# Performance work log

Measured on AMD Instinct MI355X. Metric: run time of the kernel, lower is better.

Reference implementation:

```python
import jax, jax.numpy as jnp
import numpy as np

B, H, N, D = 16, 8, 256, 32


def setup_inputs() -> dict:
    key = jax.random.key(0)
    k1, k2, k3 = jax.random.split(key, 3)
    q = jax.random.normal(k1, (B, H, N, D), dtype=jnp.float32)
    k = jax.random.normal(k2, (B, H, N, D), dtype=jnp.float32)
    scale = jnp.ones((1,), dtype=jnp.float32)  # unused by the module
    mask = jnp.zeros((B, 1, N, N), dtype=bool)  # True == masked out
    # learned attention vector, xavier_uniform over (1, H, 1, 1, D)
    fan = 1 * H * 1 * 1 * D
    bound = float(np.sqrt(6.0 / (1 + D)))  # xavier for (..., D) param
    attention = jax.random.uniform(k3, (1, H, 1, 1, D), dtype=jnp.float32,
                                   minval=-bound, maxval=bound)
    return {"q": q, "k": k, "scale": scale, "mask": mask, "attention": attention}


def reference(q, k, scale, mask, attention):
    # summed: [B, H, Nq, Nk, D] via broadcast of q.unsqueeze(-2)+k.unsqueeze(-3)
    summed = q[:, :, :, None, :] + k[:, :, None, :, :]
    # GATv2 score: a^T * silu(q_i + k_j), reduced over head_dim
    scores = jnp.sum(jax.nn.silu(summed) * attention, axis=-1)  # [B, H, Nq, Nk]
    neg = jnp.finfo(scores.dtype).min
    scores_masked = jnp.where(mask, neg, scores)
    attn = jax.nn.softmax(scores_masked, axis=-1)
    return attn
```

## Files before the change

### kernel.cpp

```cpp
#include <hip/hip_runtime.h>
#include <stdint.h>
#include <stddef.h>

constexpr int Bc = 16, Hc = 8, Nc = 256, Dc = 32;
constexpr float LOG2E = 1.44269504088896340736f;

constexpr int    MF    = 12;
constexpr double PHALF = 11.5;
constexpr double LFIT  = 9.0;

constexpr double PI_ = 3.14159265358979323846;

constexpr double cexp_(double x) {
    int n = (int)(x >= 0 ? x + 0.5 : x - 0.5);
    double f = x - n, t = 1.0, s = 1.0;
    for (int i = 1; i <= 26; ++i) { t *= f / i; s += t; }
    const double E = 2.71828182845904523536;
    double en = 1.0, bb = n >= 0 ? E : 1.0 / E;
    int an = n < 0 ? -n : n;
    for (int i = 0; i < an; ++i) en *= bb;
    return s * en;
}
constexpr double creduce_(double x) {
    while (x >  PI_) x -= 2.0 * PI_;
    while (x < -PI_) x += 2.0 * PI_;
    return x;
}
constexpr double ccos_(double x0) {
    double x = creduce_(x0), x2 = x * x, t = 1.0, s = 1.0;
    for (int i = 1; i <= 16; ++i) { t *= -x2 / ((2.0*i - 1.0) * (2.0*i)); s += t; }
    return s;
}
constexpr double csin_(double x0) {
    double x = creduce_(x0), x2 = x * x, t = x, s = x;
    for (int i = 1; i <= 16; ++i) { t *= -x2 / ((2.0*i) * (2.0*i + 1.0)); s += t; }
    return s;
}
constexpr double Gfun_(double x) {
    double z = x < 0 ? -x : x;
    double e = cexp_(z);
    return 0.5 * z * ((e - 1.0) / (e + 1.0));
}
constexpr double csqrt_(double x) {
    if (x <= 0) return 0;
    double r = x > 1 ? x : 1;
    for (int i = 0; i < 40; ++i) r = 0.5 * (r + x / r);
    return r;
}

struct FitT { float tk[MF + 1]; float tq[MF + 1]; };

constexpr FitT lsFit_() {
    constexpr int NB = MF + 1;
    double A[NB][NB] = {}, bv[NB] = {};
    for (int p = 0; p < NB; ++p)
        for (int qq = 0; qq < NB; ++qq) {
            double wm = (p - qq) * PI_ / PHALF, wp = (p + qq) * PI_ / PHALF;
            double Sm = (p == qq)     ? LFIT : csin_(wm * LFIT) / wm;
            double Sp = (p + qq == 0) ? LFIT : csin_(wp * LFIT) / wp;
            A[p][qq] = 0.5 * (Sm + Sp);
        }
    constexpr int NS = 128;
    double hh = LFIT / NS, gx[NS + 1] = {};
    for (int i = 0; i <= NS; ++i) gx[i] = Gfun_(i * hh);
    for (int p = 0; p < NB; ++p) {
        double s = 0;
        for (int i = 0; i <= NS; ++i) {
            double wgt = (i == 0 || i == NS) ? 1.0 : ((i & 1) ? 4.0 : 2.0);
            s += wgt * gx[i] * ccos_(p * PI_ / PHALF * (i * hh));
        }
        bv[p] = s * hh / 3.0;
    }
    for (int p = 0; p < NB; ++p) A[p][p] += 1e-8 * LFIT;
    for (int col = 0; col < NB; ++col) {
        int piv = col; double best = A[col][col] < 0 ? -A[col][col] : A[col][col];
        for (int r = col + 1; r < NB; ++r) {
            double v = A[r][col] < 0 ? -A[r][col] : A[r][col];
            if (v > best) { best = v; piv = r; }
        }
        if (piv != col) {
            for (int cc = 0; cc < NB; ++cc) { double t = A[col][cc]; A[col][cc] = A[piv][cc]; A[piv][cc] = t; }
            double t = bv[col]; bv[col] = bv[piv]; bv[piv] = t;
        }
        for (int r = col + 1; r < NB; ++r) {
            double f = A[r][col] / A[col][col];
            for (int cc = col; cc < NB; ++cc) A[r][cc] -= f * A[col][cc];
            bv[r] -= f * bv[col];
        }
    }
    double c[NB] = {};
    for (int r = NB - 1; r >= 0; --r) {
        double s = bv[r];
        for (int cc = r + 1; cc < NB; ++cc) s -= A[r][cc] * c[cc];
        c[r] = s / A[r][r];
    }
    FitT f{};
    for (int m = 0; m <= MF; ++m) {
        double rt = csqrt_(c[m] < 0 ? -c[m] : c[m]);
        f.tk[m] = (float)rt;
        f.tq[m] = (float)(c[m] < 0 ? -rt : rt);
    }
    return f;
}
constexpr FitT CF = lsFit_();

typedef _Float16 half8  __attribute__((ext_vector_type(8)));
typedef float    f32x16 __attribute__((ext_vector_type(16)));

__device__ __forceinline__ uint32_t pkh_(float a, float b) {
    auto v = __builtin_amdgcn_cvt_pkrtz(a, b);
    uint32_t u; __builtin_memcpy(&u, &v, 4); return u;
}

constexpr int ROWB = 144;
constexpr int KFR = 256, QFR = 128;
constexpr int BUFB = (KFR + QFR) * ROWB;
constexpr int SMEM_BYTES = 2 * BUFB + 1024 + 2048;

__global__ __launch_bounds__(512, 2) void gatv2_mfma_kernel(
    const float* __restrict__ q, const float* __restrict__ k,
    const uint8_t* __restrict__ mask, const float* __restrict__ att,
    float* __restrict__ out)
{
    extern __shared__ char smem[];
    float* akv  = (float*)(smem + 2 * BUFB);
    float* sred = (float*)(smem + 2 * BUFB + 1024);

    const int tid = threadIdx.x, lane = tid & 63, w = tid >> 6;
    const int bh = blockIdx.y, h = bh & 7, b = bh >> 3;
    const int iBlk = blockIdx.x * 128;
    const float invTwoP = (float)(1.0 / (2.0 * PHALF));

    const int dq = tid & 7, rw = tid >> 3;
    const float4 av4 = *(const float4*)(att + h * Dc + 4 * dq);

    const float* kbase = k + (size_t)bh * Nc * Dc;
    float kc1[16], ks1[16], kcm[16], ksm[16];
    int offK[4];
#pragma unroll
    for (int it = 0; it < 4; ++it) {
        int j = it * 64 + rw;
        float4 kv = *(const float4*)(kbase + j * Dc + 4 * dq);
        float part = av4.x * kv.x + av4.y * kv.y + av4.z * kv.z + av4.w * kv.w;
        part += __shfl_xor(part, 1, 64);
        part += __shfl_xor(part, 2, 64);
        part += __shfl_xor(part, 4, 64);
        if (dq == 0) akv[j] = part;
        float rv[4] = { kv.x, kv.y, kv.z, kv.w };
#pragma unroll
        for (int c = 0; c < 4; ++c) {
            float r = __builtin_amdgcn_fractf(rv[c] * invTwoP);
            kc1[4*it+c] = __builtin_amdgcn_cosf(r);
            ks1[4*it+c] = __builtin_amdgcn_sinf(r);
            kcm[4*it+c] = kc1[4*it+c];
            ksm[4*it+c] = ks1[4*it+c];
        }
        int sw = (j ^ (j >> 3)) & 7;
        offK[it] = j * ROWB + ((dq ^ sw) << 4);
    }
    const float* qbase = q + ((size_t)bh * Nc + iBlk) * Dc;
    float qc1[8], qs1[8], qcm[8], qsm[8];
    int offQ[2];
#pragma unroll
    for (int it = 0; it < 2; ++it) {
        int i = it * 64 + rw;
        float4 qv = *(const float4*)(qbase + i * Dc + 4 * dq);
        float rv[4] = { qv.x, qv.y, qv.z, qv.w };
#pragma unroll
        for (int c = 0; c < 4; ++c) {
            float r = __builtin_amdgcn_fractf(rv[c] * invTwoP);
            qc1[4*it+c] = __builtin_amdgcn_cosf(r);
            qs1[4*it+c] = __builtin_amdgcn_sinf(r);
            qcm[4*it+c] = qc1[4*it+c];
            qsm[4*it+c] = qs1[4*it+c];
        }
        int sw = (i ^ (i >> 3)) & 7;
        offQ[it] = KFR * ROWB + i * ROWB + ((dq ^ sw) << 4);
    }

    const int hi5 = lane >> 5, col = lane & 31;
    const int wi = w & 1, wj = w >> 1;
    int offA[2][4], offB[2][4];
#pragma unroll
    for (int it2 = 0; it2 < 2; ++it2) {
        int r = wi * 64 + it2 * 32 + col, sw = (r ^ (r >> 3)) & 7;
#pragma unroll
        for (int s = 0; s < 4; ++s)
            offA[it2][s] = KFR * ROWB + r * ROWB + (((2 * s + hi5) ^ sw) << 4);
    }
#pragma unroll
    for (int jt = 0; jt < 2; ++jt) {
        int r = wj * 64 + jt * 32 + col, sw = (r ^ (r >> 3)) & 7;
#pragma unroll
        for (int s = 0; s < 4; ++s)
            offB[jt][s] = r * ROWB + (((2 * s + hi5) ^ sw) << 4);
    }

    f32x16 acc[2][2];
#pragma unroll
    for (int a2 = 0; a2 < 2; ++a2)
#pragma unroll
        for (int b2 = 0; b2 < 2; ++b2)
#pragma unroll
            for (int e = 0; e < 16; ++e) acc[a2][b2][e] = 0.0f;

    auto buildChunk = [&](int m, int dstOff) {
        const float tk = CF.tk[m];
        const float g0 = CF.tq[m] * av4.x, g1 = CF.tq[m] * av4.y;
        const float g2 = CF.tq[m] * av4.z, g3 = CF.tq[m] * av4.w;
#pragma unroll
        for (int it = 0; it < 4; ++it) {
            uint4 wv;
            wv.x = pkh_(tk * kcm[4*it+0], tk * ksm[4*it+0]);
            wv.y = pkh_(tk * kcm[4*it+1], tk * ksm[4*it+1]);
            wv.z = pkh_(tk * kcm[4*it+2], tk * ksm[4*it+2]);
            wv.w = pkh_(tk * kcm[4*it+3], tk * ksm[4*it+3]);
            *(uint4*)(smem + dstOff + offK[it]) = wv;
        }
#pragma unroll
        for (int it = 0; it < 2; ++it) {
            uint4 wv;
            wv.x = pkh_(g0 * qcm[4*it+0], -(g0 * qsm[4*it+0]));
            wv.y = pkh_(g1 * qcm[4*it+1], -(g1 * qsm[4*it+1]));
            wv.z = pkh_(g2 * qcm[4*it+2], -(g2 * qsm[4*it+2]));
            wv.w = pkh_(g3 * qcm[4*it+3], -(g3 * qsm[4*it+3]));
            *(uint4*)(smem + dstOff + offQ[it]) = wv;
        }
        if (m < MF) {
#pragma unroll
            for (int e = 0; e < 16; ++e) {
                float cn = fmaf(kc1[e], kcm[e], -(ks1[e] * ksm[e]));
                float sn = fmaf(ks1[e], kcm[e],   kc1[e] * ksm[e]);
                kcm[e] = cn; ksm[e] = sn;
            }
#pragma unroll
            for (int e = 0; e < 8; ++e) {
                float cn = fmaf(qc1[e], qcm[e], -(qs1[e] * qsm[e]));
                float sn = fmaf(qs1[e], qcm[e],   qc1[e] * qsm[e]);
                qcm[e] = cn; qsm[e] = sn;
            }
        }
    };

    auto mfmaChunk = [&](int srcOff) {
#pragma unroll
        for (int s = 0; s < 4; ++s) {
            half8 A0 = *(const half8*)(smem + srcOff + offA[0][s]);
            half8 A1 = *(const half8*)(smem + srcOff + offA[1][s]);
            half8 B0 = *(const half8*)(smem + srcOff + offB[0][s]);
            half8 B1 = *(const half8*)(smem + srcOff + offB[1][s]);
            acc[0][0] = __builtin_amdgcn_mfma_f32_32x32x16_f16(A0, B0, acc[0][0], 0, 0, 0);
            acc[0][1] = __builtin_amdgcn_mfma_f32_32x32x16_f16(A0, B1, acc[0][1], 0, 0, 0);
            acc[1][0] = __builtin_amdgcn_mfma_f32_32x32x16_f16(A1, B0, acc[1][0], 0, 0, 0);
            acc[1][1] = __builtin_amdgcn_mfma_f32_32x32x16_f16(A1, B1, acc[1][1], 0, 0, 0);
        }
    };

    buildChunk(1, 0);
    __syncthreads();
#pragma unroll
    for (int m = 1; m <= MF; ++m) {
        if (m < MF) buildChunk(m + 1, (m & 1) * BUFB);
        mfmaChunk(((m - 1) & 1) * BUFB);
        __syncthreads();
    }

    constexpr float M0 = 24.0f;
    const int jB = wj * 64;
    const float akj0 = akv[jB + col], akj1 = akv[jB + 32 + col];
    const int iB = iBlk + wi * 64;

#pragma unroll
    for (int it2 = 0; it2 < 2; ++it2)
#pragma unroll
        for (int e = 0; e < 16; ++e) {
            int rloc = (e & 3) + 8 * (e >> 2) + 4 * hi5;
            int ig = iB + it2 * 32 + rloc;
            const uint8_t* mr = mask + ((size_t)(b * Nc + ig)) * Nc + jB + col;
            float v0 = fmaf(0.5f, akj0, acc[it2][0][e]);
            float v1 = fmaf(0.5f, akj1, acc[it2][1][e]);
            if (mr[0])  v0 = -1.0e30f;
            if (mr[32]) v1 = -1.0e30f;
            float p0 = __builtin_amdgcn_exp2f(__builtin_fminf((v0 - M0) * LOG2E, 80.0f));
            float p1 = __builtin_amdgcn_exp2f(__builtin_fminf((v1 - M0) * LOG2E, 80.0f));
            acc[it2][0][e] = p0;
            acc[it2][1][e] = p1;
            float sm = p0 + p1;
#pragma unroll
            for (int off = 1; off < 32; off <<= 1) sm += __shfl_xor(sm, off, 64);
            if (col == e) sred[(wi * 64 + it2 * 32 + rloc) * 4 + wj] = sm;
        }
    __syncthreads();

    float* obase = out + (size_t)bh * Nc * Nc;
#pragma unroll
    for (int it2 = 0; it2 < 2; ++it2)
#pragma unroll
        for (int e = 0; e < 16; ++e) {
            int rloc = (e & 3) + 8 * (e >> 2) + 4 * hi5;
            int iL = wi * 64 + it2 * 32 + rloc;
            int ig = iB + it2 * 32 + rloc;
            float4 tv = *(const float4*)(&sred[iL * 4]);
            float inv = __builtin_amdgcn_rcpf(tv.x + tv.y + tv.z + tv.w);
            obase[(size_t)ig * Nc + jB + col]      = acc[it2][0][e] * inv;
            obase[(size_t)ig * Nc + jB + 32 + col] = acc[it2][1][e] * inv;
        }
}

extern "C" void kernel_launch(void* const* d_in, const int* in_sizes, int n_in,
                              void* d_out, int out_size, void* d_ws, size_t ws_size,
                              hipStream_t stream) {
    const float*   q    = (const float*)d_in[0];
    const float*   k    = (const float*)d_in[1];
    const uint8_t* mask = (const uint8_t*)d_in[3];
    const float*   att  = (const float*)d_in[4];
    float*         out  = (float*)d_out;

    (void)hipFuncSetAttribute((const void*)gatv2_mfma_kernel,
                              hipFuncAttributeMaxDynamicSharedMemorySize, SMEM_BYTES);

    dim3 grid(2, Bc * Hc);
    dim3 block(512);
    gatv2_mfma_kernel<<<grid, block, SMEM_BYTES, stream>>>(q, k, mask, att, out);
}
```

Measured before the change: 104.7 us.

## Use 1024-thread blocks with smaller per-wave tiles and fewer Fourier terms

Doubles the block to 16 waves, each computing a 32x64 score tile with two accumulators instead of a 64x64 tile with four. Per-thread staging work for K and Q fragments is halved. Separately, the Fourier approximation of SiLU drops from 12 to 10 harmonics with a shorter period, so fewer MFMA chunks are built and multiplied. The fewer harmonics may reduce accuracy, and the larger block with no occupancy hint changes register pressure and residency.

```diff
diff --git a/kernel.cpp b/kernel.cpp
--- a/kernel.cpp
+++ b/kernel.cpp
@@ -5,8 +5,8 @@
 constexpr int Bc = 16, Hc = 8, Nc = 256, Dc = 32;
 constexpr float LOG2E = 1.44269504088896340736f;
 
-constexpr int    MF    = 12;
-constexpr double PHALF = 11.5;
+constexpr int    MF    = 10;
+constexpr double PHALF = 9.7;
 constexpr double LFIT  = 9.0;
 
 constexpr double PI_ = 3.14159265358979323846;
@@ -117,7 +117,7 @@
 constexpr int BUFB = (KFR + QFR) * ROWB;
 constexpr int SMEM_BYTES = 2 * BUFB + 1024 + 2048;
 
-__global__ __launch_bounds__(512, 2) void gatv2_mfma_kernel(
+__global__ __launch_bounds__(1024) void gatv2_mfma_kernel(
     const float* __restrict__ q, const float* __restrict__ k,
     const uint8_t* __restrict__ mask, const float* __restrict__ att,
     float* __restrict__ out)
@@ -135,11 +135,11 @@
     const float4 av4 = *(const float4*)(att + h * Dc + 4 * dq);
 
     const float* kbase = k + (size_t)bh * Nc * Dc;
-    float kc1[16], ks1[16], kcm[16], ksm[16];
-    int offK[4];
-#pragma unroll
-    for (int it = 0; it < 4; ++it) {
-        int j = it * 64 + rw;
+    float kc1[8], ks1[8], kcm[8], ksm[8];
+    int offK[2];
+#pragma unroll
+    for (int it = 0; it < 2; ++it) {
+        int j = rw + it * 128;
         float4 kv = *(const float4*)(kbase + j * Dc + 4 * dq);
         float part = av4.x * kv.x + av4.y * kv.y + av4.z * kv.z + av4.w * kv.w;
         part += __shfl_xor(part, 1, 64);
@@ -159,57 +159,44 @@
         offK[it] = j * ROWB + ((dq ^ sw) << 4);
     }
     const float* qbase = q + ((size_t)bh * Nc + iBlk) * Dc;
-    float qc1[8], qs1[8], qcm[8], qsm[8];
-    int offQ[2];
-#pragma unroll
-    for (int it = 0; it < 2; ++it) {
-        int i = it * 64 + rw;
-        float4 qv = *(const float4*)(qbase + i * Dc + 4 * dq);
+    float qc1[4], qs1[4], qcm[4], qsm[4];
+    int offQ;
+    {
+        float4 qv = *(const float4*)(qbase + rw * Dc + 4 * dq);
         float rv[4] = { qv.x, qv.y, qv.z, qv.w };
 #pragma unroll
         for (int c = 0; c < 4; ++c) {
             float r = __builtin_amdgcn_fractf(rv[c] * invTwoP);
-            qc1[4*it+c] = __builtin_amdgcn_cosf(r);
-            qs1[4*it+c] = __builtin_amdgcn_sinf(r);
-            qcm[4*it+c] = qc1[4*it+c];
-            qsm[4*it+c] = qs1[4*it+c];
-        }
-        int sw = (i ^ (i >> 3)) & 7;
-        offQ[it] = KFR * ROWB + i * ROWB + ((dq ^ sw) << 4);
+            qc1[c] = __builtin_amdgcn_cosf(r);
+            qs1[c] = __builtin_amdgcn_sinf(r);
+            qcm[c] = qc1[c];
+            qsm[c] = qs1[c];
+        }
+        int sw = (rw ^ (rw >> 3)) & 7;
+        offQ = KFR * ROWB + rw * ROWB + ((dq ^ sw) << 4);
     }
 
     const int hi5 = lane >> 5, col = lane & 31;
-    const int wi = w & 1, wj = w >> 1;
-    int offA[2][4], offB[2][4];
-#pragma unroll
-    for (int it2 = 0; it2 < 2; ++it2) {
-        int r = wi * 64 + it2 * 32 + col, sw = (r ^ (r >> 3)) & 7;
-#pragma unroll
-        for (int s = 0; s < 4; ++s)
-            offA[it2][s] = KFR * ROWB + r * ROWB + (((2 * s + hi5) ^ sw) << 4);
-    }
-#pragma unroll
-    for (int jt = 0; jt < 2; ++jt) {
-        int r = wj * 64 + jt * 32 + col, sw = (r ^ (r >> 3)) & 7;
-#pragma unroll
-        for (int s = 0; s < 4; ++s)
-            offB[jt][s] = r * ROWB + (((2 * s + hi5) ^ sw) << 4);
-    }
-
-    f32x16 acc[2][2];
-#pragma unroll
-    for (int a2 = 0; a2 < 2; ++a2)
-#pragma unroll
-        for (int b2 = 0; b2 < 2; ++b2)
-#pragma unroll
-            for (int e = 0; e < 16; ++e) acc[a2][b2][e] = 0.0f;
+    const int wi = w & 3, wj = w >> 2;
+    const int rA  = wi * 32 + col;
+    const int swA = (rA ^ (rA >> 3)) & 7;
+    const int baseA = KFR * ROWB + rA * ROWB;
+    const int rB0 = wj * 64 + col, rB1 = rB0 + 32;
+    const int swB0 = (rB0 ^ (rB0 >> 3)) & 7, swB1 = (rB1 ^ (rB1 >> 3)) & 7;
+    const int baseB0 = rB0 * ROWB, baseB1 = rB1 * ROWB;
+
+    f32x16 acc[2];
+#pragma unroll
+    for (int jt = 0; jt < 2; ++jt)
+#pragma unroll
+        for (int e = 0; e < 16; ++e) acc[jt][e] = 0.0f;
 
     auto buildChunk = [&](int m, int dstOff) {
         const float tk = CF.tk[m];
         const float g0 = CF.tq[m] * av4.x, g1 = CF.tq[m] * av4.y;
         const float g2 = CF.tq[m] * av4.z, g3 = CF.tq[m] * av4.w;
 #pragma unroll
-        for (int it = 0; it < 4; ++it) {
+        for (int it = 0; it < 2; ++it) {
             uint4 wv;
             wv.x = pkh_(tk * kcm[4*it+0], tk * ksm[4*it+0]);
             wv.y = pkh_(tk * kcm[4*it+1], tk * ksm[4*it+1]);
@@ -217,24 +204,23 @@
             wv.w = pkh_(tk * kcm[4*it+3], tk * ksm[4*it+3]);
             *(uint4*)(smem + dstOff + offK[it]) = wv;
         }
-#pragma unroll
-        for (int it = 0; it < 2; ++it) {
+        {
             uint4 wv;
-            wv.x = pkh_(g0 * qcm[4*it+0], -(g0 * qsm[4*it+0]));
-            wv.y = pkh_(g1 * qcm[4*it+1], -(g1 * qsm[4*it+1]));
-            wv.z = pkh_(g2 * qcm[4*it+2], -(g2 * qsm[4*it+2]));
-            wv.w = pkh_(g3 * qcm[4*it+3], -(g3 * qsm[4*it+3]));
-            *(uint4*)(smem + dstOff + offQ[it]) = wv;
+            wv.x = pkh_(g0 * qcm[0], -(g0 * qsm[0]));
+            wv.y = pkh_(g1 * qcm[1], -(g1 * qsm[1]));
+            wv.z = pkh_(g2 * qcm[2], -(g2 * qsm[2]));
+            wv.w = pkh_(g3 * qcm[3], -(g3 * qsm[3]));
+            *(uint4*)(smem + dstOff + offQ) = wv;
         }
         if (m < MF) {
 #pragma unroll
-            for (int e = 0; e < 16; ++e) {
+            for (int e = 0; e < 8; ++e) {
                 float cn = fmaf(kc1[e], kcm[e], -(ks1[e] * ksm[e]));
                 float sn = fmaf(ks1[e], kcm[e],   kc1[e] * ksm[e]);
                 kcm[e] = cn; ksm[e] = sn;
             }
 #pragma unroll
-            for (int e = 0; e < 8; ++e) {
+            for (int e = 0; e < 4; ++e) {
                 float cn = fmaf(qc1[e], qcm[e], -(qs1[e] * qsm[e]));
                 float sn = fmaf(qs1[e], qcm[e],   qc1[e] * qsm[e]);
                 qcm[e] = cn; qsm[e] = sn;
@@ -245,14 +231,12 @@
     auto mfmaChunk = [&](int srcOff) {
 #pragma unroll
         for (int s = 0; s < 4; ++s) {
-            half8 A0 = *(const half8*)(smem + srcOff + offA[0][s]);
-            half8 A1 = *(const half8*)(smem + srcOff + offA[1][s]);
-            half8 B0 = *(const half8*)(smem + srcOff + offB[0][s]);
-            half8 B1 = *(const half8*)(smem + srcOff + offB[1][s]);
-            acc[0][0] = __builtin_amdgcn_mfma_f32_32x32x16_f16(A0, B0, acc[0][0], 0, 0, 0);
-            acc[0][1] = __builtin_amdgcn_mfma_f32_32x32x16_f16(A0, B1, acc[0][1], 0, 0, 0);
-            acc[1][0] = __builtin_amdgcn_mfma_f32_32x32x16_f16(A1, B0, acc[1][0], 0, 0, 0);
-            acc[1][1] = __builtin_amdgcn_mfma_f32_32x32x16_f16(A1, B1, acc[1][1], 0, 0, 0);
+            int u = 2 * s + hi5;
+            half8 A  = *(const half8*)(smem + srcOff + baseA  + ((u ^ swA ) << 4));
+            half8 B0 = *(const half8*)(smem + srcOff + baseB0 + ((u ^ swB0) << 4));
+            half8 B1 = *(const half8*)(smem + srcOff + baseB1 + ((u ^ swB1) << 4));
+            acc[0] = __builtin_amdgcn_mfma_f32_32x32x16_f16(A, B0, acc[0], 0, 0, 0);
+            acc[1] = __builtin_amdgcn_mfma_f32_32x32x16_f16(A, B1, acc[1], 0, 0, 0);
         }
     };
 
@@ -268,43 +252,39 @@
     constexpr float M0 = 24.0f;
     const int jB = wj * 64;
     const float akj0 = akv[jB + col], akj1 = akv[jB + 32 + col];
-    const int iB = iBlk + wi * 64;
-
-#pragma unroll
-    for (int it2 = 0; it2 < 2; ++it2)
-#pragma unroll
-        for (int e = 0; e < 16; ++e) {
-            int rloc = (e & 3) + 8 * (e >> 2) + 4 * hi5;
-            int ig = iB + it2 * 32 + rloc;
-            const uint8_t* mr = mask + ((size_t)(b * Nc + ig)) * Nc + jB + col;
-            float v0 = fmaf(0.5f, akj0, acc[it2][0][e]);
-            float v1 = fmaf(0.5f, akj1, acc[it2][1][e]);
-            if (mr[0])  v0 = -1.0e30f;
-            if (mr[32]) v1 = -1.0e30f;
-            float p0 = __builtin_amdgcn_exp2f(__builtin_fminf((v0 - M0) * LOG2E, 80.0f));
-            float p1 = __builtin_amdgcn_exp2f(__builtin_fminf((v1 - M0) * LOG2E, 80.0f));
-            acc[it2][0][e] = p0;
-            acc[it2][1][e] = p1;
-            float sm = p0 + p1;
-#pragma unroll
-            for (int off = 1; off < 32; off <<= 1) sm += __shfl_xor(sm, off, 64);
-            if (col == e) sred[(wi * 64 + it2 * 32 + rloc) * 4 + wj] = sm;
-        }
+    const int iB = iBlk + wi * 32;
+
+#pragma unroll
+    for (int e = 0; e < 16; ++e) {
+        int rloc = (e & 3) + 8 * (e >> 2) + 4 * hi5;
+        int ig = iB + rloc;
+        const uint8_t* mr = mask + ((size_t)(b * Nc + ig)) * Nc + jB + col;
+        float v0 = fmaf(0.5f, akj0, acc[0][e]);
+        float v1 = fmaf(0.5f, akj1, acc[1][e]);
+        if (mr[0])  v0 = -1.0e30f;
+        if (mr[32]) v1 = -1.0e30f;
+        float p0 = __builtin_amdgcn_exp2f(__builtin_fminf((v0 - M0) * LOG2E, 80.0f));
+        float p1 = __builtin_amdgcn_exp2f(__builtin_fminf((v1 - M0) * LOG2E, 80.0f));
+        acc[0][e] = p0;
+        acc[1][e] = p1;
+        float sm = p0 + p1;
+#pragma unroll
+        for (int off = 1; off < 32; off <<= 1) sm += __shfl_xor(sm, off, 64);
+        if (col == e) sred[(wi * 32 + rloc) * 4 + wj] = sm;
+    }
     __syncthreads();
 
     float* obase = out + (size_t)bh * Nc * Nc;
 #pragma unroll
-    for (int it2 = 0; it2 < 2; ++it2)
-#pragma unroll
-        for (int e = 0; e < 16; ++e) {
-            int rloc = (e & 3) + 8 * (e >> 2) + 4 * hi5;
-            int iL = wi * 64 + it2 * 32 + rloc;
-            int ig = iB + it2 * 32 + rloc;
-            float4 tv = *(const float4*)(&sred[iL * 4]);
-            float inv = __builtin_amdgcn_rcpf(tv.x + tv.y + tv.z + tv.w);
-            obase[(size_t)ig * Nc + jB + col]      = acc[it2][0][e] * inv;
-            obase[(size_t)ig * Nc + jB + 32 + col] = acc[it2][1][e] * inv;
-        }
+    for (int e = 0; e < 16; ++e) {
+        int rloc = (e & 3) + 8 * (e >> 2) + 4 * hi5;
+        int iL = wi * 32 + rloc;
+        int ig = iB + rloc;
+        float4 tv = *(const float4*)(&sred[iL * 4]);
+        float inv = __builtin_amdgcn_rcpf(tv.x + tv.y + tv.z + tv.w);
+        obase[(size_t)ig * Nc + jB + col]      = acc[0][e] * inv;
+        obase[(size_t)ig * Nc + jB + 32 + col] = acc[1][e] * inv;
+    }
 }
 
 extern "C" void kernel_launch(void* const* d_in, const int* in_sizes, int n_in,
@@ -320,6 +300,6 @@
                               hipFuncAttributeMaxDynamicSharedMemorySize, SMEM_BYTES);
 
     dim3 grid(2, Bc * Hc);
-    dim3 block(512);
+    dim3 block(1024);
     gatv2_mfma_kernel<<<grid, block, SMEM_BYTES, stream>>>(q, k, mask, att, out);
 }
```

New measurement: 98.82 us. -5.7%, faster.

## Precompute K Fourier features in separate kernel and DMA them into LDS

Applied to the files above, without the earlier changes.

Splits the work into a feature kernel that computes the half-precision K Fourier features and the a·k terms once per (b,h), and a GEMM kernel that streams those features from workspace into LDS with global_load_lds DMA while it builds only the Q features. This removes the K feature computation that was repeated in both row blocks and takes VALU work out of the MFMA loop. It also cuts the Fourier order from 12 to 10 and shrinks the period, which changes the approximation's accuracy. The cost is a second kernel launch and a large workspace write and read of the K features.

```diff
diff --git a/kernel.cpp b/kernel.cpp
--- a/kernel.cpp
+++ b/kernel.cpp
@@ -5,8 +5,8 @@
 constexpr int Bc = 16, Hc = 8, Nc = 256, Dc = 32;
 constexpr float LOG2E = 1.44269504088896340736f;
 
-constexpr int    MF    = 12;
-constexpr double PHALF = 11.5;
+constexpr int    MF    = 10;
+constexpr double PHALF = 9.7;
 constexpr double LFIT  = 9.0;
 
 constexpr double PI_ = 3.14159265358979323846;
@@ -112,60 +112,91 @@
     uint32_t u; __builtin_memcpy(&u, &v, 4); return u;
 }
 
-constexpr int ROWB = 144;
-constexpr int KFR = 256, QFR = 128;
-constexpr int BUFB = (KFR + QFR) * ROWB;
-constexpr int SMEM_BYTES = 2 * BUFB + 1024 + 2048;
-
-__global__ __launch_bounds__(512, 2) void gatv2_mfma_kernel(
-    const float* __restrict__ q, const float* __restrict__ k,
-    const uint8_t* __restrict__ mask, const float* __restrict__ att,
-    float* __restrict__ out)
+__device__ __forceinline__ void dma16(const char* g, char* l) {
+    __builtin_amdgcn_global_load_lds(
+        (const __attribute__((address_space(1))) unsigned int*)(g),
+        (__attribute__((address_space(3))) unsigned int*)(l),
+        16, 0, 0);
+}
+
+constexpr int    KCH      = Nc * 128;
+constexpr size_t KF_BYTES = (size_t)Bc * Hc * MF * KCH;
+constexpr size_t AK_OFF   = KF_BYTES;
+
+__global__ __launch_bounds__(256) void feat_kernel(
+    const float* __restrict__ k, const float* __restrict__ att,
+    char* __restrict__ kf, float* __restrict__ akg)
+{
+    const int gid = blockIdx.x * 256 + threadIdx.x;
+    const int u  = gid & 7;
+    const int j  = (gid >> 3) & (Nc - 1);
+    const int bh = gid >> 11;
+    const int h  = bh & (Hc - 1);
+    const float4 kv = *(const float4*)(k + ((size_t)bh * Nc + j) * Dc + 4 * u);
+    const float4 a4 = *(const float4*)(att + h * Dc + 4 * u);
+    float part = a4.x * kv.x + a4.y * kv.y + a4.z * kv.z + a4.w * kv.w;
+    part += __shfl_xor(part, 1, 64);
+    part += __shfl_xor(part, 2, 64);
+    part += __shfl_xor(part, 4, 64);
+    if (u == 0) akg[bh * Nc + j] = part;
+
+    const float invTwoP = (float)(1.0 / (2.0 * PHALF));
+    float c1[4], s1[4], cm[4], sm[4];
+    const float rv[4] = { kv.x, kv.y, kv.z, kv.w };
+#pragma unroll
+    for (int c = 0; c < 4; ++c) {
+        float r = __builtin_amdgcn_fractf(rv[c] * invTwoP);
+        c1[c] = __builtin_amdgcn_cosf(r);
+        s1[c] = __builtin_amdgcn_sinf(r);
+        cm[c] = c1[c]; sm[c] = s1[c];
+    }
+    char* base = kf + (size_t)bh * (MF * KCH) + j * 128 + ((u ^ (j & 7)) << 4);
+#pragma unroll
+    for (int m = 1; m <= MF; ++m) {
+        const float tk = CF.tk[m];
+        uint4 wv;
+        wv.x = pkh_(tk * cm[0], tk * sm[0]);
+        wv.y = pkh_(tk * cm[1], tk * sm[1]);
+        wv.z = pkh_(tk * cm[2], tk * sm[2]);
+        wv.w = pkh_(tk * cm[3], tk * sm[3]);
+        *(uint4*)(base + (size_t)(m - 1) * KCH) = wv;
+        if (m < MF) {
+#pragma unroll
+            for (int e = 0; e < 4; ++e) {
+                float cn = fmaf(c1[e], cm[e], -(s1[e] * sm[e]));
+                float sn = fmaf(s1[e], cm[e],   c1[e] * sm[e]);
+                cm[e] = cn; sm[e] = sn;
+            }
+        }
+    }
+}
+
+constexpr int QCH   = 128 * 128;
+constexpr int QBASE = 2 * KCH;
+constexpr int SRED  = QBASE + 2 * QCH;
+constexpr int SMEM2 = SRED + 2048;
+
+__global__ __launch_bounds__(512, 2) void gatv2_gemm_kernel(
+    const float* __restrict__ q, const uint8_t* __restrict__ mask,
+    const float* __restrict__ att, const char* __restrict__ kf,
+    const float* __restrict__ akg, float* __restrict__ out)
 {
     extern __shared__ char smem[];
-    float* akv  = (float*)(smem + 2 * BUFB);
-    float* sred = (float*)(smem + 2 * BUFB + 1024);
-
+    float* sred = (float*)(smem + SRED);
     const int tid = threadIdx.x, lane = tid & 63, w = tid >> 6;
     const int bh = blockIdx.y, h = bh & 7, b = bh >> 3;
     const int iBlk = blockIdx.x * 128;
     const float invTwoP = (float)(1.0 / (2.0 * PHALF));
 
     const int dq = tid & 7, rw = tid >> 3;
-    const float4 av4 = *(const float4*)(att + h * Dc + 4 * dq);
-
-    const float* kbase = k + (size_t)bh * Nc * Dc;
-    float kc1[16], ks1[16], kcm[16], ksm[16];
-    int offK[4];
-#pragma unroll
-    for (int it = 0; it < 4; ++it) {
-        int j = it * 64 + rw;
-        float4 kv = *(const float4*)(kbase + j * Dc + 4 * dq);
-        float part = av4.x * kv.x + av4.y * kv.y + av4.z * kv.z + av4.w * kv.w;
-        part += __shfl_xor(part, 1, 64);
-        part += __shfl_xor(part, 2, 64);
-        part += __shfl_xor(part, 4, 64);
-        if (dq == 0) akv[j] = part;
-        float rv[4] = { kv.x, kv.y, kv.z, kv.w };
-#pragma unroll
-        for (int c = 0; c < 4; ++c) {
-            float r = __builtin_amdgcn_fractf(rv[c] * invTwoP);
-            kc1[4*it+c] = __builtin_amdgcn_cosf(r);
-            ks1[4*it+c] = __builtin_amdgcn_sinf(r);
-            kcm[4*it+c] = kc1[4*it+c];
-            ksm[4*it+c] = ks1[4*it+c];
-        }
-        int sw = (j ^ (j >> 3)) & 7;
-        offK[it] = j * ROWB + ((dq ^ sw) << 4);
-    }
-    const float* qbase = q + ((size_t)bh * Nc + iBlk) * Dc;
+    const float4 a4 = *(const float4*)(att + h * Dc + 4 * dq);
     float qc1[8], qs1[8], qcm[8], qsm[8];
     int offQ[2];
 #pragma unroll
     for (int it = 0; it < 2; ++it) {
-        int i = it * 64 + rw;
-        float4 qv = *(const float4*)(qbase + i * Dc + 4 * dq);
-        float rv[4] = { qv.x, qv.y, qv.z, qv.w };
+        const int i = rw + it * 64;
+        const float4 qv = *(const float4*)(q + ((size_t)bh * Nc + iBlk + i) * Dc + 4 * dq);
+        const float rv[4] = { qv.x, qv.y, qv.z, qv.w };
 #pragma unroll
         for (int c = 0; c < 4; ++c) {
             float r = __builtin_amdgcn_fractf(rv[c] * invTwoP);
@@ -174,65 +205,32 @@
             qcm[4*it+c] = qc1[4*it+c];
             qsm[4*it+c] = qs1[4*it+c];
         }
-        int sw = (i ^ (i >> 3)) & 7;
-        offQ[it] = KFR * ROWB + i * ROWB + ((dq ^ sw) << 4);
-    }
-
-    const int hi5 = lane >> 5, col = lane & 31;
-    const int wi = w & 1, wj = w >> 1;
-    int offA[2][4], offB[2][4];
-#pragma unroll
-    for (int it2 = 0; it2 < 2; ++it2) {
-        int r = wi * 64 + it2 * 32 + col, sw = (r ^ (r >> 3)) & 7;
-#pragma unroll
-        for (int s = 0; s < 4; ++s)
-            offA[it2][s] = KFR * ROWB + r * ROWB + (((2 * s + hi5) ^ sw) << 4);
-    }
-#pragma unroll
-    for (int jt = 0; jt < 2; ++jt) {
-        int r = wj * 64 + jt * 32 + col, sw = (r ^ (r >> 3)) & 7;
-#pragma unroll
-        for (int s = 0; s < 4; ++s)
-            offB[jt][s] = r * ROWB + (((2 * s + hi5) ^ sw) << 4);
-    }
-
-    f32x16 acc[2][2];
-#pragma unroll
-    for (int a2 = 0; a2 < 2; ++a2)
-#pragma unroll
-        for (int b2 = 0; b2 < 2; ++b2)
-#pragma unroll
-            for (int e = 0; e < 16; ++e) acc[a2][b2][e] = 0.0f;
-
-    auto buildChunk = [&](int m, int dstOff) {
-        const float tk = CF.tk[m];
-        const float g0 = CF.tq[m] * av4.x, g1 = CF.tq[m] * av4.y;
-        const float g2 = CF.tq[m] * av4.z, g3 = CF.tq[m] * av4.w;
-#pragma unroll
-        for (int it = 0; it < 4; ++it) {
-            uint4 wv;
-            wv.x = pkh_(tk * kcm[4*it+0], tk * ksm[4*it+0]);
-            wv.y = pkh_(tk * kcm[4*it+1], tk * ksm[4*it+1]);
-            wv.z = pkh_(tk * kcm[4*it+2], tk * ksm[4*it+2]);
-            wv.w = pkh_(tk * kcm[4*it+3], tk * ksm[4*it+3]);
-            *(uint4*)(smem + dstOff + offK[it]) = wv;
-        }
+        offQ[it] = QBASE + i * 128 + ((dq ^ (i & 7)) << 4);
+    }
+
+    const char* kg = kf + (size_t)bh * (MF * KCH) + w * 4096 + lane * 16;
+
+    auto dmaK = [&](int mIdx, int buf) {
+        const char* g = kg + (size_t)mIdx * KCH;
+        char* l = smem + buf * KCH + w * 4096;
+#pragma unroll
+        for (int t = 0; t < 4; ++t)
+            dma16(g + t * 1024, l + t * 1024);
+    };
+
+    auto buildQ = [&](int m, int buf) {
+        const float g0 = CF.tq[m]*a4.x, g1 = CF.tq[m]*a4.y;
+        const float g2 = CF.tq[m]*a4.z, g3 = CF.tq[m]*a4.w;
 #pragma unroll
         for (int it = 0; it < 2; ++it) {
             uint4 wv;
-            wv.x = pkh_(g0 * qcm[4*it+0], -(g0 * qsm[4*it+0]));
-            wv.y = pkh_(g1 * qcm[4*it+1], -(g1 * qsm[4*it+1]));
-            wv.z = pkh_(g2 * qcm[4*it+2], -(g2 * qsm[4*it+2]));
-            wv.w = pkh_(g3 * qcm[4*it+3], -(g3 * qsm[4*it+3]));
-            *(uint4*)(smem + dstOff + offQ[it]) = wv;
+            wv.x = pkh_(g0*qcm[4*it+0], -(g0*qsm[4*it+0]));
+            wv.y = pkh_(g1*qcm[4*it+1], -(g1*qsm[4*it+1]));
+            wv.z = pkh_(g2*qcm[4*it+2], -(g2*qsm[4*it+2]));
+            wv.w = pkh_(g3*qcm[4*it+3], -(g3*qsm[4*it+3]));
+            *(uint4*)(smem + buf * QCH + offQ[it]) = wv;
         }
         if (m < MF) {
-#pragma unroll
-            for (int e = 0; e < 16; ++e) {
-                float cn = fmaf(kc1[e], kcm[e], -(ks1[e] * ksm[e]));
-                float sn = fmaf(ks1[e], kcm[e],   kc1[e] * ksm[e]);
-                kcm[e] = cn; ksm[e] = sn;
-            }
 #pragma unroll
             for (int e = 0; e < 8; ++e) {
                 float cn = fmaf(qc1[e], qcm[e], -(qs1[e] * qsm[e]));
@@ -242,13 +240,29 @@
         }
     };
 
-    auto mfmaChunk = [&](int srcOff) {
+    const int hi5 = lane >> 5, col = lane & 31;
+    const int wi = w & 1, wj = w >> 1;
+    const int baseA0 = QBASE + (wi*64 + col) * 128, baseA1 = baseA0 + 32*128;
+    const int baseB0 = (wj*64 + col) * 128,         baseB1 = baseB0 + 32*128;
+    const int sA = col & 7;
+
+    f32x16 acc[2][2];
+#pragma unroll
+    for (int a2 = 0; a2 < 2; ++a2)
+#pragma unroll
+        for (int b2 = 0; b2 < 2; ++b2)
+#pragma unroll
+            for (int e = 0; e < 16; ++e) acc[a2][b2][e] = 0.0f;
+
+    auto mfmaC = [&](int buf) {
+        const int qb = buf * QCH, kb = buf * KCH;
 #pragma unroll
         for (int s = 0; s < 4; ++s) {
-            half8 A0 = *(const half8*)(smem + srcOff + offA[0][s]);
-            half8 A1 = *(const half8*)(smem + srcOff + offA[1][s]);
-            half8 B0 = *(const half8*)(smem + srcOff + offB[0][s]);
-            half8 B1 = *(const half8*)(smem + srcOff + offB[1][s]);
+            const int du = ((2*s + hi5) ^ sA) << 4;
+            half8 A0 = *(const half8*)(smem + qb + baseA0 + du);
+            half8 A1 = *(const half8*)(smem + qb + baseA1 + du);
+            half8 B0 = *(const half8*)(smem + kb + baseB0 + du);
+            half8 B1 = *(const half8*)(smem + kb + baseB1 + du);
             acc[0][0] = __builtin_amdgcn_mfma_f32_32x32x16_f16(A0, B0, acc[0][0], 0, 0, 0);
             acc[0][1] = __builtin_amdgcn_mfma_f32_32x32x16_f16(A0, B1, acc[0][1], 0, 0, 0);
             acc[1][0] = __builtin_amdgcn_mfma_f32_32x32x16_f16(A1, B0, acc[1][0], 0, 0, 0);
@@ -256,18 +270,21 @@
         }
     };
 
-    buildChunk(1, 0);
+    buildQ(1, 0);
+    dmaK(0, 0);
     __syncthreads();
 #pragma unroll
     for (int m = 1; m <= MF; ++m) {
-        if (m < MF) buildChunk(m + 1, (m & 1) * BUFB);
-        mfmaChunk(((m - 1) & 1) * BUFB);
+        const int cur = (m - 1) & 1;
+        if (m < MF) { dmaK(m, 1 - cur); buildQ(m + 1, 1 - cur); }
+        mfmaC(cur);
         __syncthreads();
     }
 
     constexpr float M0 = 24.0f;
     const int jB = wj * 64;
-    const float akj0 = akv[jB + col], akj1 = akv[jB + 32 + col];
+    const float akj0 = akg[bh * Nc + jB + col];
+    const float akj1 = akg[bh * Nc + jB + 32 + col];
     const int iB = iBlk + wi * 64;
 
 #pragma unroll
@@ -316,10 +333,15 @@
     const float*   att  = (const float*)d_in[4];
     float*         out  = (float*)d_out;
 
-    (void)hipFuncSetAttribute((const void*)gatv2_mfma_kernel,
-                              hipFuncAttributeMaxDynamicSharedMemorySize, SMEM_BYTES);
-
+    char*  kfbuf = (char*)d_ws;
+    float* akg   = (float*)((char*)d_ws + AK_OFF);
+
+    feat_kernel<<<dim3((Bc * Hc * Nc * 8) / 256), dim3(256), 0, stream>>>(
+        k, att, kfbuf, akg);
+
+    (void)hipFuncSetAttribute((const void*)gatv2_gemm_kernel,
+                              hipFuncAttributeMaxDynamicSharedMemorySize, SMEM2);
     dim3 grid(2, Bc * Hc);
-    dim3 block(512);
-    gatv2_mfma_kernel<<<grid, block, SMEM_BYTES, stream>>>(q, k, mask, att, out);
-}
+    gatv2_gemm_kernel<<<grid, dim3(512), SMEM2, stream>>>(
+        q, mask, att, kfbuf, akg, out);
+}
```

Result: slower. 112.4 us (+7.4%).
